# Kernel optimization log

Hardware: AMD Instinct MI355X
Metric: run time of the kernel (lower is better)

## Reference

```python
import jax, jax.numpy as jnp
import numpy as np

EMBED_DIM = 256
NUM_HEADS = 8
HEAD_DIM = EMBED_DIM // NUM_HEADS
SCALE = HEAD_DIM ** -0.5  # note: scale uses head_dim even though attention is over full D
EPS = 1e-12  # torch F.normalize eps


def setup_inputs() -> dict:
    key = jax.random.key(0)
    k1, k2, k3 = jax.random.split(key, 3)
    B, Nq, Nk, D = 4, 4096, 4096, EMBED_DIM
    return {
        "query": jax.random.normal(k1, (B, Nq, D), dtype=jnp.float32),
        "key": jax.random.normal(k2, (B, Nk, D), dtype=jnp.float32),
        "value": jax.random.normal(k3, (B, Nk, D), dtype=jnp.float32),
    }


def _l2_normalize(x):
    # matches torch.nn.functional.normalize(x, dim=-1): x / max(||x||, eps)
    n = jnp.linalg.norm(x, axis=-1, keepdims=True)
    return x / jnp.maximum(n, EPS)


def reference(query, key, value):
    q = _l2_normalize(query)          # (B, Nq, D)
    k = _l2_normalize(key)            # (B, Nk, D)
    scores = jnp.einsum("bqd,bkd->bqk", q, k) * SCALE  # (B, Nq, Nk) cosine sims
    attn = jax.nn.softmax(scores, axis=-1)
    return jnp.einsum("bqk,bkd->bqd", attn, value)     # (B, Nq, D)
```

## Files before the change

kernel.cpp:

```cpp
#include <hip/hip_runtime.h>


#define NQ 4096
#define DIM 256
#define NROWS 16384
#define BM 64
#define BN 64
#define KSPLIT 2
#define NITER 32
#define PSTRIDE 68
#define QSTRIDE 264

typedef __attribute__((ext_vector_type(8))) short bf16x8;
typedef __attribute__((ext_vector_type(4))) float f32x4;
typedef __attribute__((ext_vector_type(16))) float f32x16;

__device__ __forceinline__ unsigned short f2bf(float f) {
  unsigned int u = __float_as_uint(f);
  u += 0x7fffu + ((u >> 16) & 1u);
  return (unsigned short)(u >> 16);
}

__device__ __forceinline__ float bf2f(unsigned short h) {
  return __uint_as_float((unsigned int)h << 16);
}

__device__ __forceinline__ unsigned int pack2bf(float a, float b) {
  unsigned int ua = __float_as_uint(a) + 0x8000u;
  unsigned int ub = __float_as_uint(b) + 0x8000u;
  return __builtin_amdgcn_perm(ub, ua, 0x07060302u);
}

__device__ __forceinline__ void gload16(const void* g, void* l) {
  __builtin_amdgcn_global_load_lds(
      (const __attribute__((address_space(1))) unsigned int*)g,
      (__attribute__((address_space(3))) unsigned int*)l, 16, 0, 0);
}

__global__ __launch_bounds__(256) void prep(
    const float* __restrict__ K, const float* __restrict__ V,
    unsigned short* __restrict__ Kfm, unsigned short* __restrict__ Vfm)
{
  __shared__ unsigned short vt[32 * 264];
  const int blk = blockIdx.x, tid = threadIdx.x;
  const int wave = tid >> 6, lane = tid & 63;
  if (blk < 512) {
    const int kt2 = blk;
    const int kt = kt2 >> 1, h = kt2 & 1;
    #pragma unroll
    for (int i = 0; i < 8; i++) {
      const int r = wave*8 + i;
      float4 v = *(const float4*)(K + ((size_t)kt2*32 + r) * DIM + lane * 4);
      float ss = v.x*v.x + v.y*v.y + v.z*v.z + v.w*v.w;
      #pragma unroll
      for (int off = 1; off < 64; off <<= 1) ss += __shfl_xor(ss, off, 64);
      float scale = 1.0f / fmaxf(sqrtf(ss), 1e-12f);
      ushort4 o;
      o.x = f2bf(v.x*scale); o.y = f2bf(v.y*scale);
      o.z = f2bf(v.z*scale); o.w = f2bf(v.w*scale);
      *(ushort4*)(vt + r*264 + lane*4) = o;
    }
    __syncthreads();
    #pragma unroll
    for (int s = 0; s < 4; s++) {
      const int ch = tid + 256*s;
      const int c = ch >> 5, r = ch & 31;
      const int n = h*32 + r;
      bf16x8 val = *(const bf16x8*)(vt + r*264 + c*8);
      *(bf16x8*)(Kfm + (size_t)kt*16384 + (size_t)(c*64 + n)*8) = val;
    }
  } else {
    const int NS = blk - 512;
    #pragma unroll
    for (int i = 0; i < 4; i++) {
      const int e = tid + 256*i;
      const int nl = e >> 6, d = (e & 63) * 4;
      float4 v = *(const float4*)(V + ((size_t)NS*16 + nl)*DIM + d);
      ushort4 o;
      o.x = f2bf(v.x); o.y = f2bf(v.y); o.z = f2bf(v.z); o.w = f2bf(v.w);
      *(ushort4*)(vt + nl*264 + d) = o;
    }
    __syncthreads();
    #pragma unroll
    for (int i = 0; i < 2; i++) {
      const int ch = tid + 256*i;
      const int db = ch >> 6, ln = ch & 63;
      const int row0 = (ln >> 5) * 8, dd = db*32 + (ln & 31);
      ushort4 a, b;
      a.x = vt[(row0+0)*264 + dd]; a.y = vt[(row0+1)*264 + dd];
      a.z = vt[(row0+2)*264 + dd]; a.w = vt[(row0+3)*264 + dd];
      b.x = vt[(row0+4)*264 + dd]; b.y = vt[(row0+5)*264 + dd];
      b.z = vt[(row0+6)*264 + dd]; b.w = vt[(row0+7)*264 + dd];
      size_t base = ((size_t)(NS*8 + db)*64 + ln)*8;
      *(ushort4*)(Vfm + base)     = a;
      *(ushort4*)(Vfm + base + 4) = b;
    }
  }
}

__global__ __launch_bounds__(256, 2) void attn(
    const float* __restrict__ Qg,
    const unsigned short* __restrict__ Kfm,
    const unsigned short* __restrict__ Vfm,
    unsigned short* __restrict__ Opart, float* __restrict__ lpart)
{
  __shared__ unsigned short Klds[2][32 * 64 * 8];
  __shared__ unsigned short Plds[BM * PSTRIDE];

  const int tid = threadIdx.x, wave = tid >> 6, lane = tid & 63;
  const int l15 = lane & 15, l4 = lane >> 4;
  const int blk = blockIdx.x;
  const int g = blk & 7, qt = blk >> 3;
  const int b = g >> 1, ks = g & 1;
  const int Rq0 = b*NQ + qt*BM;
  const int n0base = b*NQ + ks*(NQ/KSPLIT);
  const int mi = wave & 1, ni = wave >> 1;

  {
    unsigned short* Qlds = &Klds[0][0];
    #pragma unroll
    for (int i = 0; i < 16; i++) {
      const int r = wave*16 + i;
      float4 v = *(const float4*)(Qg + (size_t)(Rq0 + r)*DIM + lane*4);
      float ss = v.x*v.x + v.y*v.y + v.z*v.z + v.w*v.w;
      #pragma unroll
      for (int off = 1; off < 64; off <<= 1) ss += __shfl_xor(ss, off, 64);
      float scale = (0.17677669529663687f * 1.4426950408889634f)
                    / fmaxf(sqrtf(ss), 1e-12f);
      ushort4 o;
      o.x = f2bf(v.x*scale); o.y = f2bf(v.y*scale);
      o.z = f2bf(v.z*scale); o.w = f2bf(v.w*scale);
      *(ushort4*)(Qlds + r*QSTRIDE + lane*4) = o;
    }
  }
  __syncthreads();

  bf16x8 qf[2][8];
  #pragma unroll
  for (int mt = 0; mt < 2; mt++) {
    const unsigned short* qrow = &Klds[0][0] + (mi*32 + mt*16 + l15)*QSTRIDE + l4*8;
    #pragma unroll
    for (int kg = 0; kg < 8; kg++)
      qf[mt][kg] = *(const bf16x8*)(qrow + kg*32);
  }
  __syncthreads();

  f32x16 oacc[2][2] = {};
  float lacc[2] = {};

  auto stage = [&](int kt_) {
    unsigned short* dst = &Klds[kt_ & 1][0];
    const unsigned short* src = Kfm + (size_t)((n0base + kt_*BN) >> 6) * (32*64*8);
    #pragma unroll
    for (int jj = 0; jj < 4; jj++) {
      const int c = wave*8 + jj*2;
      gload16(src + (size_t)c*512 + lane*8,     dst + (size_t)c*512);
      gload16(src + (size_t)(c+1)*512 + lane*8, dst + (size_t)(c+1)*512);
    }
  };

  stage(0);

  for (int kt = 0; kt < NITER; kt++) {
    __syncthreads();

    if (kt + 1 < NITER) stage(kt + 1);
    __builtin_amdgcn_sched_barrier(0);

    const unsigned short* kb = &Klds[kt & 1][0];

    f32x4 sacc[2][2] = {};
    #pragma unroll
    for (int kg = 0; kg < 8; kg++) {
      bf16x8 kf[2];
      #pragma unroll
      for (int nt = 0; nt < 2; nt++) {
        const int nrow = ni*32 + nt*16 + l15;
        const int c = kg*4 + l4;
        kf[nt] = *(const bf16x8*)(kb + ((size_t)(c*64 + nrow))*8);
      }
      __builtin_amdgcn_s_setprio(1);
      #pragma unroll
      for (int nt = 0; nt < 2; nt++)
        #pragma unroll
        for (int mt = 0; mt < 2; mt++)
          sacc[nt][mt] = __builtin_amdgcn_mfma_f32_16x16x32_bf16(
              kf[nt], qf[mt][kg], sacc[nt][mt], 0, 0, 0);
      __builtin_amdgcn_s_setprio(0);
    }

    #pragma unroll
    for (int nt = 0; nt < 2; nt++)
      #pragma unroll
      for (int mt = 0; mt < 2; mt++) {
        float p0 = __builtin_amdgcn_exp2f(sacc[nt][mt][0]);
        float p1 = __builtin_amdgcn_exp2f(sacc[nt][mt][1]);
        float p2 = __builtin_amdgcn_exp2f(sacc[nt][mt][2]);
        float p3 = __builtin_amdgcn_exp2f(sacc[nt][mt][3]);
        lacc[mt] += (p0 + p1) + (p2 + p3);
        uint2 pk;
        pk.x = pack2bf(p0, p1);
        pk.y = pack2bf(p2, p3);
        const int m = mi*32 + mt*16 + l15;
        const int n = ni*32 + nt*16 + 4*l4;
        *(uint2*)(Plds + m*PSTRIDE + n) = pk;
      }

    asm volatile("s_waitcnt lgkmcnt(0)" ::: "memory");
    __builtin_amdgcn_s_barrier();
    __builtin_amdgcn_sched_barrier(0);

    const int NB0 = (n0base + kt*BN) >> 4;
    bf16x8 pf[2][2], vf[2][2];
    #pragma unroll
    for (int mt2 = 0; mt2 < 2; mt2++)
      pf[0][mt2] = *(const bf16x8*)(Plds + (mt2*32 + (lane & 31))*PSTRIDE
                                    + 8*(lane >> 5));
    #pragma unroll
    for (int dt = 0; dt < 2; dt++)
      vf[0][dt] = *(const bf16x8*)(Vfm + ((size_t)(NB0*8 + wave*2 + dt)*64 + lane)*8);
    #pragma unroll
    for (int kstep = 0; kstep < 4; kstep++) {
      const int cb = kstep & 1;
      if (kstep < 3) {
        #pragma unroll
        for (int mt2 = 0; mt2 < 2; mt2++)
          pf[cb^1][mt2] = *(const bf16x8*)(Plds + (mt2*32 + (lane & 31))*PSTRIDE
                                           + (kstep+1)*16 + 8*(lane >> 5));
        #pragma unroll
        for (int dt = 0; dt < 2; dt++)
          vf[cb^1][dt] = *(const bf16x8*)(Vfm
              + ((size_t)((NB0 + kstep + 1)*8 + wave*2 + dt)*64 + lane)*8);
      }
      __builtin_amdgcn_s_setprio(1);
      #pragma unroll
      for (int mt2 = 0; mt2 < 2; mt2++)
        #pragma unroll
        for (int dt = 0; dt < 2; dt++)
          oacc[mt2][dt] = __builtin_amdgcn_mfma_f32_32x32x16_bf16(
              pf[cb][mt2], vf[cb][dt], oacc[mt2][dt], 0, 0, 0);
      __builtin_amdgcn_s_setprio(0);
    }
  }

  #pragma unroll
  for (int mt = 0; mt < 2; mt++) {
    float s = lacc[mt];
    s += __shfl_xor(s, 16, 64);
    s += __shfl_xor(s, 32, 64);
    if (l4 == 0)
      lpart[(size_t)(ks*2 + ni)*NROWS + Rq0 + mi*32 + mt*16 + l15] = s;
  }

  #pragma unroll
  for (int mt2 = 0; mt2 < 2; mt2++)
    #pragma unroll
    for (int dt = 0; dt < 2; dt++)
      #pragma unroll
      for (int reg = 0; reg < 16; reg++) {
        const int m = mt2*32 + 4*(lane >> 5) + (reg & 3) + 8*(reg >> 2);
        const int d = wave*64 + dt*32 + (lane & 31);
        Opart[((size_t)(ks*NROWS + Rq0 + m))*DIM + d] = f2bf(oacc[mt2][dt][reg]);
      }
}

__global__ __launch_bounds__(256) void combine(
    const unsigned short* __restrict__ Opart, const float* __restrict__ lpart,
    float* __restrict__ out)
{
  const size_t idx = (size_t)blockIdx.x*256 + threadIdx.x;
  const size_t e = idx*4;
  const int R = (int)(e >> 8);
  ushort4 o0 = *(const ushort4*)(Opart + e);
  ushort4 o1 = *(const ushort4*)(Opart + (size_t)NROWS*DIM + e);
  float ls = lpart[R] + lpart[NROWS + R] + lpart[2*NROWS + R] + lpart[3*NROWS + R];
  float inv = 1.0f / ls;
  float4 o;
  o.x = (bf2f(o0.x) + bf2f(o1.x))*inv;
  o.y = (bf2f(o0.y) + bf2f(o1.y))*inv;
  o.z = (bf2f(o0.z) + bf2f(o1.z))*inv;
  o.w = (bf2f(o0.w) + bf2f(o1.w))*inv;
  *(float4*)(out + e) = o;
}

extern "C" void kernel_launch(void* const* d_in, const int* in_sizes, int n_in,
                              void* d_out, int out_size, void* d_ws, size_t ws_size,
                              hipStream_t stream) {
  const float* Q = (const float*)d_in[0];
  const float* K = (const float*)d_in[1];
  const float* V = (const float*)d_in[2];
  char* ws = (char*)d_ws;
  unsigned short* Kfm   = (unsigned short*)(ws);
  unsigned short* Vfm   = (unsigned short*)(ws + 8388608);
  unsigned short* Opart = (unsigned short*)(ws + 16777216);
  float* lpart = (float*)(ws + 33554432);

  prep<<<1536, 256, 0, stream>>>(K, V, Kfm, Vfm);
  attn<<<512, 256, 0, stream>>>(Q, Kfm, Vfm, Opart, lpart);
  combine<<<4096, 256, 0, stream>>>(Opart, lpart, (float*)d_out);
}
```

Baseline: 172.0 us.

## Fuse split-K combine into attention kernel via last-block atomic counter

Removes the separate combine launch. Each attention block atomically bumps a per-(batch, q-tile) counter after writing its partial output, and whichever of the two split blocks arrives second merges both partials into the final output. The counters are zeroed in the prep kernel. This saves a kernel launch and a full pass over the partial buffers, but adds threadfences, an atomic, and serialized combine work on the last-arriving blocks.

```diff
diff --git a/kernel.cpp b/kernel.cpp
--- a/kernel.cpp
+++ b/kernel.cpp
@@ -39,11 +39,13 @@
 
 __global__ __launch_bounds__(256) void prep(
     const float* __restrict__ K, const float* __restrict__ V,
-    unsigned short* __restrict__ Kfm, unsigned short* __restrict__ Vfm)
+    unsigned short* __restrict__ Kfm, unsigned short* __restrict__ Vfm,
+    int* __restrict__ cnt)
 {
   __shared__ unsigned short vt[32 * 264];
   const int blk = blockIdx.x, tid = threadIdx.x;
   const int wave = tid >> 6, lane = tid & 63;
+  if (blk == 0) cnt[tid] = 0;
   if (blk < 512) {
     const int kt2 = blk;
     const int kt = kt2 >> 1, h = kt2 & 1;
@@ -102,10 +104,12 @@
     const float* __restrict__ Qg,
     const unsigned short* __restrict__ Kfm,
     const unsigned short* __restrict__ Vfm,
-    unsigned short* __restrict__ Opart, float* __restrict__ lpart)
+    unsigned short* __restrict__ Opart, float* __restrict__ lpart,
+    int* __restrict__ cnt, float* __restrict__ out)
 {
   __shared__ unsigned short Klds[2][32 * 64 * 8];
   __shared__ unsigned short Plds[BM * PSTRIDE];
+  __shared__ int last_s;
 
   const int tid = threadIdx.x, wave = tid >> 6, lane = tid & 63;
   const int l15 = lane & 15, l4 = lane >> 4;
@@ -262,25 +266,32 @@
         const int d = wave*64 + dt*32 + (lane & 31);
         Opart[((size_t)(ks*NROWS + Rq0 + m))*DIM + d] = f2bf(oacc[mt2][dt][reg]);
       }
-}
-
-__global__ __launch_bounds__(256) void combine(
-    const unsigned short* __restrict__ Opart, const float* __restrict__ lpart,
-    float* __restrict__ out)
-{
-  const size_t idx = (size_t)blockIdx.x*256 + threadIdx.x;
-  const size_t e = idx*4;
-  const int R = (int)(e >> 8);
-  ushort4 o0 = *(const ushort4*)(Opart + e);
-  ushort4 o1 = *(const ushort4*)(Opart + (size_t)NROWS*DIM + e);
-  float ls = lpart[R] + lpart[NROWS + R] + lpart[2*NROWS + R] + lpart[3*NROWS + R];
-  float inv = 1.0f / ls;
-  float4 o;
-  o.x = (bf2f(o0.x) + bf2f(o1.x))*inv;
-  o.y = (bf2f(o0.y) + bf2f(o1.y))*inv;
-  o.z = (bf2f(o0.z) + bf2f(o1.z))*inv;
-  o.w = (bf2f(o0.w) + bf2f(o1.w))*inv;
-  *(float4*)(out + e) = o;
+
+  __threadfence();
+  __syncthreads();
+  if (tid == 0)
+    last_s = atomicAdd(&cnt[(g >> 1)*64 + qt], 1);
+  __syncthreads();
+  if (last_s == 1) {
+    __threadfence();
+    #pragma unroll
+    for (int i = 0; i < 16; i++) {
+      const int e4 = tid + 256*i;
+      const size_t e = (size_t)Rq0*DIM + (size_t)e4*4;
+      const int R = Rq0 + (e4 >> 6);
+      float ls = lpart[R] + lpart[NROWS + R]
+               + lpart[2*NROWS + R] + lpart[3*NROWS + R];
+      float inv = 1.0f / ls;
+      ushort4 o0 = *(const ushort4*)(Opart + e);
+      ushort4 o1 = *(const ushort4*)(Opart + (size_t)NROWS*DIM + e);
+      float4 o;
+      o.x = (bf2f(o0.x) + bf2f(o1.x))*inv;
+      o.y = (bf2f(o0.y) + bf2f(o1.y))*inv;
+      o.z = (bf2f(o0.z) + bf2f(o1.z))*inv;
+      o.w = (bf2f(o0.w) + bf2f(o1.w))*inv;
+      *(float4*)(out + e) = o;
+    }
+  }
 }
 
 extern "C" void kernel_launch(void* const* d_in, const int* in_sizes, int n_in,
@@ -294,8 +305,8 @@
   unsigned short* Vfm   = (unsigned short*)(ws + 8388608);
   unsigned short* Opart = (unsigned short*)(ws + 16777216);
   float* lpart = (float*)(ws + 33554432);
-
-  prep<<<1536, 256, 0, stream>>>(K, V, Kfm, Vfm);
-  attn<<<512, 256, 0, stream>>>(Q, Kfm, Vfm, Opart, lpart);
-  combine<<<4096, 256, 0, stream>>>(Opart, lpart, (float*)d_out);
-}
+  int* cnt     = (int*)(ws + 33554432 + 262144);
+
+  prep<<<1536, 256, 0, stream>>>(K, V, Kfm, Vfm, cnt);
+  attn<<<512, 256, 0, stream>>>(Q, Kfm, Vfm, Opart, lpart, cnt, (float*)d_out);
+}
```

New measurement: 267.3 us. 55.4% more time.
